# Kernel tuning notes

Hardware: AMD Instinct MI355X
Metric: run time of the kernel (lower is better)

Reference implementation:

```python
import jax, jax.numpy as jnp
import numpy as np

B, CH, H, W = 8, 1024, 64, 64
FD = 128            # feature_dim
NUM_K, POOL_PER_K = 64, 32
POOL = NUM_K * POOL_PER_K  # 2048


def setup_inputs() -> dict:
    key = jax.random.key(0)
    ks = jax.random.split(key, 7)
    s = 0.02  # keep logits in a sane range for softmax
    return {
        "x": jax.random.normal(ks[0], (B, CH, H, W), jnp.float32),
        "w_theta": jax.random.normal(ks[1], (FD, CH), jnp.float32) * s,
        "w_phi": jax.random.normal(ks[2], (FD, CH), jnp.float32) * s,
        "w_g": jax.random.normal(ks[3], (FD, CH), jnp.float32) * s,
        "w_o": jax.random.normal(ks[4], (CH, FD), jnp.float32) * s,
        "gamma": jnp.ones((1,), jnp.float32),
        "concept_pool": jax.random.uniform(ks[5], (FD, POOL), jnp.float32),
    }


def reference(x, w_theta, w_phi, w_g, w_o, gamma, concept_pool):
    b, c, h, w = x.shape
    n = h * w
    xf = x.reshape(b, c, n)                                   # [B, C, N]
    # 1x1 conv projections as matmuls
    theta = jnp.einsum('fc,bcn->bfn', w_theta, xf)            # [B, FD, N]
    # --- concept-codebook cross attention: queries attend over pool entries ---
    cp_logits = jnp.einsum('bfn,fp->bnp', theta, concept_pool)  # [B, N, P]
    cp_attn = jax.nn.softmax(cp_logits, axis=-1)
    pooled = jnp.einsum('bnp,fp->bfn', cp_attn, concept_pool)   # [B, FD, N]
    # --- standard self-attention branch (use_sa=True) ---
    phi = jnp.einsum('fc,bcn->bfn', w_phi, xf)                # [B, FD, N]
    g = jnp.einsum('fc,bcn->bfn', w_g, xf)                    # [B, FD, N]
    sa_logits = jnp.einsum('bfn,bfm->bnm', theta, phi)        # [B, N, N]
    sa_attn = jax.nn.softmax(sa_logits, axis=-1)
    sa_out = jnp.einsum('bnm,bfm->bfn', sa_attn, g)           # [B, FD, N]
    # combine, output 1x1 conv, gamma-scaled residual
    feat = pooled + sa_out
    out = jnp.einsum('cf,bfn->bcn', w_o, feat).reshape(b, c, h, w)
    return gamma[0] * out + x
```

## Files before the change

### kernel.cpp

```cpp
#include <hip/hip_runtime.h>

typedef unsigned short u16;
typedef unsigned int u32;
typedef float f32x4 __attribute__((ext_vector_type(4)));
typedef short s16x8 __attribute__((ext_vector_type(8)));

#define B_ 8
#define C_ 1024
#define N_ 4096
#define FD_ 128
#define P_ 2048
#define LOG2E 1.4426950408889634f

__device__ __forceinline__ u16 f2bf(float f) {
  u32 u = __float_as_uint(f);
  u32 r = (u + 0x7fffu + ((u >> 16) & 1u)) >> 16;
  return (u16)r;
}
__device__ __forceinline__ u32 pkbf(float a, float b) {
  u32 r;
  asm("v_cvt_pk_bf16_f32 %0, %1, %2" : "=v"(r) : "v"(a), "v"(b));
  return r;
}
__device__ __forceinline__ float lo16(u32 u) { return __uint_as_float(u << 16); }
__device__ __forceinline__ float hi16(u32 u) { return __uint_as_float(u & 0xffff0000u); }
__device__ __forceinline__ float bf2f(u16 u) { return __uint_as_float(((u32)u) << 16); }

#define AS1 __attribute__((address_space(1)))
#define AS3 __attribute__((address_space(3)))
__device__ __forceinline__ void gl16(const void* g, void* l) {
  __builtin_amdgcn_global_load_lds((AS1 const u32*)g, (AS3 u32*)l, 16, 0, 0);
}

__device__ __forceinline__ int tau32(int c) {
  return ((c & 4) << 2) + ((c & 24) >> 1) + (c & 3);
}

__global__ __launch_bounds__(256) void prep_kernel(
    const float* __restrict__ wth, const float* __restrict__ wph,
    const float* __restrict__ wg, const float* __restrict__ wo,
    const float* __restrict__ pool,
    u16* __restrict__ wcat, u16* __restrict__ wo_bf,
    u16* __restrict__ pool_k, u16* __restrict__ pool_vt) {
  int idx = blockIdx.x * 256 + threadIdx.x;
  if (idx < 393216) {
    int o = idx;
    int e = o & 7, hi2 = (o >> 3) & 3, lo2 = (o >> 5) & 15;
    int ft = (o >> 9) & 7, ks = (o >> 12) & 1, kk2 = (o >> 13) & 15;
    int y = o >> 17;
    int c = kk2 * 64 + ks * 32 + hi2 * 8 + e;
    int fj = y * 128 + ft * 16 + lo2;
    float v = (fj < 128) ? wth[fj * 1024 + c]
              : (fj < 256 ? wph[(fj - 128) * 1024 + c]
                          : wg[(fj - 256) * 1024 + c]);
    wcat[idx] = f2bf(v);
  } else if (idx < 524288) {
    int i = idx - 393216;
    wo_bf[i] = f2bf(wo[i]);
  } else if (idx < 786432) {
    int i = idx - 524288;
    int p = i >> 7, f = i & 127;
    pool_k[i] = f2bf(pool[f * 2048 + p]);
  } else if (idx < 1048576) {
    int j = idx - 786432;
    int tile = j >> 12, r = j & 4095;
    int ch = r >> 10, f = (r >> 3) & 127, kk = r & 7;
    pool_vt[j] = f2bf(pool[f * 2048 + tile * 32 + tau32(ch * 8 + kk)]);
  }
}

#define SWZ(r) ((((r) + ((r) >> 3)) & 7) << 4)
__global__ __launch_bounds__(256, 2) void proj_kernel(
    const float* __restrict__ x, const u16* __restrict__ wcat,
    u16* __restrict__ q_t, u16* __restrict__ k_t, u16* __restrict__ gvt) {
  __shared__ __align__(16) char sm[34816];
  float* ot = (float*)sm;
  const int tid = threadIdx.x;
  const int w = tid >> 6, lane = tid & 63, lo = lane & 15, hi = lane >> 4;
  const int bid = blockIdx.x;
  const int xcd = bid & 7, slot = bid >> 3;
  const int y = slot % 3, t8 = slot / 3;
  const int tile = t8 * 8 + xcd;
  const int b = tile >> 5, n0 = (tile & 31) * 128;

  const float* xb = x + (size_t)b * (C_ * N_) + n0;
  const u16* wy = wcat + y * 131072;
  const int cq = tid >> 4, nq = tid & 15;

  f32x4 acc[2][8];
#pragma unroll
  for (int s = 0; s < 2; ++s)
#pragma unroll
    for (int ft = 0; ft < 8; ++ft)
#pragma unroll
      for (int j = 0; j < 4; ++j) acc[s][ft][j] = 0.f;

  float4 xa[8];
  s16x8 bA[8], bB[8];

#define LOADX(c0)                                                        \
  {                                                                      \
    _Pragma("unroll") for (int i = 0; i < 4; ++i) {                      \
      const float* p = xb + (size_t)((c0) + cq * 4 + i) * N_ + nq * 8;   \
      xa[i * 2] = *(const float4*)p;                                     \
      xa[i * 2 + 1] = *(const float4*)(p + 4);                           \
    }                                                                    \
  }
#define STOREA(bufsel)                                                   \
  {                                                                      \
    char* ab = sm + (bufsel)*16384;                                      \
    _Pragma("unroll") for (int j = 0; j < 8; ++j) {                      \
      float v0 = xa[0 + (j >> 2)][j & 3];                                \
      float v1 = xa[2 + (j >> 2)][j & 3];                                \
      float v2 = xa[4 + (j >> 2)][j & 3];                                \
      float v3 = xa[6 + (j >> 2)][j & 3];                                \
      uint2 pk;                                                          \
      pk.x = pkbf(v0, v1);                                               \
      pk.y = pkbf(v2, v3);                                               \
      int r = nq * 8 + j;                                                \
      *(uint2*)(ab + r * 128 + ((cq * 8) ^ SWZ(r))) = pk;                \
    }                                                                    \
  }
#define LOADB(dst, kk2, ks)                                              \
  {                                                                      \
    _Pragma("unroll") for (int ft = 0; ft < 8; ++ft) dst[ft] =           \
        *(const s16x8*)(wy + (((kk2)*2 + (ks)) * 8 + ft) * 512 +         \
                        lo * 32 + hi * 8);                               \
  }
#define COMPUTE(bufsel, ks, bf)                                          \
  {                                                                      \
    const char* ab = sm + (bufsel)*16384;                                \
    _Pragma("unroll") for (int s = 0; s < 2; ++s) {                      \
      int r = w * 32 + s * 16 + lo;                                      \
      s16x8 af = *(const s16x8*)(ab + r * 128 +                          \
                                 (((ks)*64 + hi * 16) ^ SWZ(r)));        \
      _Pragma("unroll") for (int ft = 0; ft < 8; ++ft) acc[s][ft] =      \
          __builtin_amdgcn_mfma_f32_16x16x32_bf16(af, bf[ft],            \
                                                  acc[s][ft], 0, 0, 0);  \
    }                                                                    \
  }

  LOADX(0);
  LOADB(bA, 0, 0);
  STOREA(0);
  __syncthreads();

  for (int k = 0; k < 16; ++k) {
    if (k < 15) LOADX((k + 1) * 64);
    LOADB(bB, k, 1);
    COMPUTE(k & 1, 0, bA);
    if (k < 15) LOADB(bA, k + 1, 0);
    COMPUTE(k & 1, 1, bB);
    if (k < 15) STOREA((k & 1) ^ 1);
    __syncthreads();
  }

  const float sc = (y == 0) ? LOG2E : 1.f;
#pragma unroll
  for (int hn = 0; hn < 2; ++hn) {
    if ((w >> 1) == hn) {
#pragma unroll
      for (int s = 0; s < 2; ++s)
#pragma unroll
        for (int ft = 0; ft < 8; ++ft)
#pragma unroll
          for (int j = 0; j < 4; ++j)
            ot[((w & 1) * 32 + s * 16 + hi * 4 + j) * 136 + ft * 16 + lo] =
                acc[s][ft][j] * sc;
    }
    __syncthreads();
    if (y < 2) {
      u16* arr = (y == 0) ? q_t : k_t;
      const int row = tid >> 2, fc = (tid & 3) * 32;
      u16* dst = arr + (size_t)(b * N_ + n0 + hn * 64 + row) * FD_ + fc;
      const float* sp = ot + row * 136 + fc;
#pragma unroll
      for (int k2 = 0; k2 < 4; ++k2) {
        s16x8 vv;
#pragma unroll
        for (int i = 0; i < 8; ++i) vv[i] = (short)f2bf(sp[k2 * 8 + i]);
        *(s16x8*)(dst + k2 * 8) = vv;
      }
    } else {
      const int f = tid >> 1, sel = tid & 1;
      const int t2 = (n0 >> 5) + hn * 2 + sel;
      u16* dstb = gvt + ((size_t)(b * 128 + t2) * 4) * 1024;
#pragma unroll
      for (int ch = 0; ch < 4; ++ch) {
        s16x8 vv;
#pragma unroll
        for (int kk = 0; kk < 8; ++kk) {
          int row = sel * 32 + tau32(ch * 8 + kk);
          vv[kk] = (short)f2bf(ot[row * 136 + f]);
        }
        *(s16x8*)(dstb + (ch * 128 + f) * 8) = vv;
      }
    }
    __syncthreads();
  }
#undef LOADX
#undef STOREA
#undef LOADB
#undef COMPUTE
}

__global__ __launch_bounds__(256, 3) void attn_kernel(
    const u16* __restrict__ q_t, const u16* __restrict__ k_t,
    const u16* __restrict__ pool_k, const u16* __restrict__ pool_vt,
    const u16* __restrict__ gvt, u16* __restrict__ feat1,
    u16* __restrict__ pooled, u16* __restrict__ po1, u16* __restrict__ po2,
    float* __restrict__ lse, const int NS) {
  __shared__ __align__(16) char smem[32768];
  char* kB = smem;
  char* vB = smem + 16384;

  const int tid = threadIdx.x;
  const int w = tid >> 6, lane = tid & 63, lo = lane & 15, hi = lane >> 4;
  const int b = blockIdx.x & 7;
  const int nt = (blockIdx.x >> 3) & 31;
  const int sid = (int)(blockIdx.x >> 8);
  const int n0 = nt * 128;
  const int ntiles = (NS == 3) ? 64 : 192;
  const bool DOPOOL = (NS == 1);

  const int k_dr = lane >> 4, k_cb = (lane & 15) * 16;
  const int sw = (lo & 7) << 4;

  const char* ktb = (const char*)(k_t + (size_t)b * N_ * FD_);
  const char* vtb = (const char*)(gvt + (size_t)b * 128 * 4096);
  const char* kseg0;
  const char* vseg0;
  const char* kseg1 = ktb;
  const char* vseg1 = vtb;
  if (NS == 3 && sid > 0) {
    kseg0 = ktb + (size_t)(sid - 1) * 64 * 8192;
    vseg0 = vtb + (size_t)(sid - 1) * 64 * 8192;
  } else {
    kseg0 = (const char*)pool_k;
    vseg0 = (const char*)pool_vt;
  }

  s16x8 q[2][4];
#pragma unroll
  for (int qf = 0; qf < 2; ++qf) {
    const u16* qbase = q_t + (size_t)(b * N_ + n0 + w * 32 + qf * 16 + lo) * FD_;
#pragma unroll
    for (int kk = 0; kk < 4; ++kk) q[qf][kk] = *(const s16x8*)(qbase + kk * 32 + hi * 8);
  }

  float m_r = -__builtin_inff();
  float l_r[2] = {0.f, 0.f};
  f32x4 o[2][8];
  u32 o1p[2][8][2];
#pragma unroll
  for (int qf = 0; qf < 2; ++qf)
#pragma unroll
    for (int ft = 0; ft < 8; ++ft) {
#pragma unroll
      for (int j = 0; j < 4; ++j) o[qf][ft][j] = 0.f;
      o1p[qf][ft][0] = 0u;
      o1p[qf][ft][1] = 0u;
    }

#define STAGE(i, bufsel)                                                   \
  {                                                                        \
    const char* kg = ((i) < 64) ? kseg0 + (size_t)(i)*8192                 \
                                : kseg1 + (size_t)((i)-64) * 8192;         \
    const char* vg = ((i) < 64) ? vseg0 + (size_t)(i)*8192                 \
                                : vseg1 + (size_t)((i)-64) * 8192;         \
    char* kl = kB + (bufsel)*8192;                                         \
    char* vl = vB + (bufsel)*8192;                                         \
    _Pragma("unroll") for (int cc2 = 0; cc2 < 2; ++cc2) {                  \
      int c = w * 2 + cc2;                                                 \
      int rl = c * 4 + k_dr;                                               \
      gl16(kg + rl * 256 + (k_cb ^ ((rl & 7) << 4)), kl + c * 1024);       \
      gl16(vg + c * 1024 + lane * 16, vl + c * 1024);                      \
    }                                                                      \
  }

  STAGE(0, 0);
  __syncthreads();

  int buf = 0;
  for (int i = 0; i < ntiles; ++i) {
    if (i + 1 < ntiles) STAGE(i + 1, buf ^ 1);
    if (DOPOOL && i == 64) {
#pragma unroll
      for (int qf = 0; qf < 2; ++qf) {
        float lq = l_r[qf];
        lq += __shfl_xor(lq, 16);
        lq += __shfl_xor(lq, 32);
        float inv = __builtin_amdgcn_rcpf(lq);
#pragma unroll
        for (int ft = 0; ft < 8; ++ft) {
          o1p[qf][ft][0] = pkbf(o[qf][ft][0] * inv, o[qf][ft][1] * inv);
          o1p[qf][ft][1] = pkbf(o[qf][ft][2] * inv, o[qf][ft][3] * inv);
#pragma unroll
          for (int j = 0; j < 4; ++j) o[qf][ft][j] = 0.f;
        }
        l_r[qf] = 0.f;
      }
      m_r = -__builtin_inff();
    }

    const char* kbc = kB + buf * 8192;
    const char* vbc = vB + buf * 8192;

    f32x4 s[2][2];
#pragma unroll
    for (int qf = 0; qf < 2; ++qf)
#pragma unroll
      for (int t = 0; t < 2; ++t)
#pragma unroll
        for (int j = 0; j < 4; ++j) s[qf][t][j] = 0.f;
#pragma unroll
    for (int kk = 0; kk < 4; ++kk) {
      const int cb = (kk * 64 + hi * 16) ^ sw;
      s16x8 kf0 = *(const s16x8*)(kbc + lo * 256 + cb);
      s16x8 kf1 = *(const s16x8*)(kbc + (16 + lo) * 256 + cb);
#pragma unroll
      for (int qf = 0; qf < 2; ++qf) {
        s[qf][0] = __builtin_amdgcn_mfma_f32_16x16x32_bf16(kf0, q[qf][kk], s[qf][0], 0, 0, 0);
        s[qf][1] = __builtin_amdgcn_mfma_f32_16x16x32_bf16(kf1, q[qf][kk], s[qf][1], 0, 0, 0);
      }
    }
    float tm = fmaxf(
        fmaxf(fmaxf(fmaxf(s[0][0][0], s[0][0][1]), fmaxf(s[0][0][2], s[0][0][3])),
              fmaxf(fmaxf(s[0][1][0], s[0][1][1]), fmaxf(s[0][1][2], s[0][1][3]))),
        fmaxf(fmaxf(fmaxf(s[1][0][0], s[1][0][1]), fmaxf(s[1][0][2], s[1][0][3])),
              fmaxf(fmaxf(s[1][1][0], s[1][1][1]), fmaxf(s[1][1][2], s[1][1][3]))));
    tm = fmaxf(tm, __shfl_xor(tm, 16));
    tm = fmaxf(tm, __shfl_xor(tm, 32));
    if (__any(tm - m_r > 11.5f)) {
      float mn = fmaxf(m_r, tm);
      float al = exp2f(m_r - mn);
      m_r = mn;
      l_r[0] *= al;
      l_r[1] *= al;
#pragma unroll
      for (int qf = 0; qf < 2; ++qf)
#pragma unroll
        for (int ft = 0; ft < 8; ++ft)
#pragma unroll
          for (int j = 0; j < 4; ++j) o[qf][ft][j] *= al;
    }
    union Frag { u32 u[4]; s16x8 v; };
    Frag pb[2];
#pragma unroll
    for (int qf = 0; qf < 2; ++qf) {
      float rs = 0.f;
#pragma unroll
      for (int t = 0; t < 2; ++t)
#pragma unroll
        for (int j = 0; j < 4; ++j) {
          float p = exp2f(s[qf][t][j] - m_r);
          s[qf][t][j] = p;
          rs += p;
        }
      l_r[qf] += rs;
      pb[qf].u[0] = pkbf(s[qf][0][0], s[qf][0][1]);
      pb[qf].u[1] = pkbf(s[qf][0][2], s[qf][0][3]);
      pb[qf].u[2] = pkbf(s[qf][1][0], s[qf][1][1]);
      pb[qf].u[3] = pkbf(s[qf][1][2], s[qf][1][3]);
    }
#pragma unroll
    for (int ft = 0; ft < 8; ++ft) {
      const int f = ft * 16 + lo;
      s16x8 vf = *(const s16x8*)(vbc + hi * 2048 + f * 16);
      o[0][ft] = __builtin_amdgcn_mfma_f32_16x16x32_bf16(vf, pb[0].v, o[0][ft], 0, 0, 0);
      o[1][ft] = __builtin_amdgcn_mfma_f32_16x16x32_bf16(vf, pb[1].v, o[1][ft], 0, 0, 0);
    }
    __syncthreads();
    buf ^= 1;
  }
#undef STAGE

#pragma unroll
  for (int qf = 0; qf < 2; ++qf) {
    float lq = l_r[qf];
    lq += __shfl_xor(lq, 16);
    lq += __shfl_xor(lq, 32);
    float inv = __builtin_amdgcn_rcpf(lq);
    const size_t row = (size_t)(b * N_ + n0 + w * 32 + qf * 16 + lo);
    if (NS == 1) {
#pragma unroll
      for (int ft = 0; ft < 8; ++ft) {
        float v0 = lo16(o1p[qf][ft][0]) + o[qf][ft][0] * inv;
        float v1 = hi16(o1p[qf][ft][0]) + o[qf][ft][1] * inv;
        float v2 = lo16(o1p[qf][ft][1]) + o[qf][ft][2] * inv;
        float v3 = hi16(o1p[qf][ft][1]) + o[qf][ft][3] * inv;
        uint2 st = {pkbf(v0, v1), pkbf(v2, v3)};
        *(uint2*)(feat1 + row * FD_ + ft * 16 + hi * 4) = st;
      }
    } else {
      u16* dst = (sid == 0) ? pooled : ((sid == 1) ? po1 : po2);
#pragma unroll
      for (int ft = 0; ft < 8; ++ft) {
        uint2 st = {pkbf(o[qf][ft][0] * inv, o[qf][ft][1] * inv),
                    pkbf(o[qf][ft][2] * inv, o[qf][ft][3] * inv)};
        *(uint2*)(dst + row * FD_ + ft * 16 + hi * 4) = st;
      }
      if (sid > 0 && hi == 0) lse[(sid - 1) * 32768 + row] = m_r + log2f(lq);
    }
  }
}

__global__ __launch_bounds__(256) void merge_kernel(
    const u16* __restrict__ pooled, const u16* __restrict__ po1,
    const u16* __restrict__ po2, const float* __restrict__ lse,
    u16* __restrict__ featq) {
  const int tid = threadIdx.x;
  const int n = blockIdx.x * 32 + (tid >> 3);
  const int fc = (tid & 7) * 16;
  float l1 = lse[n], l2 = lse[32768 + n];
  float mx = fmaxf(l1, l2);
  float w1 = exp2f(l1 - mx), w2 = exp2f(l2 - mx);
  float dn = __builtin_amdgcn_rcpf(w1 + w2);
  float a1 = w1 * dn, a2 = w2 * dn;
  const size_t base = (size_t)n * FD_ + fc;
#pragma unroll
  for (int h = 0; h < 2; ++h) {
    s16x8 xp = *(const s16x8*)(pooled + base + h * 8);
    s16x8 x1 = *(const s16x8*)(po1 + base + h * 8);
    s16x8 x2 = *(const s16x8*)(po2 + base + h * 8);
    s16x8 r;
#pragma unroll
    for (int i = 0; i < 8; ++i) {
      float v = bf2f((u16)xp[i]) + bf2f((u16)x1[i]) * a1 + bf2f((u16)x2[i]) * a2;
      r[i] = (short)f2bf(v);
    }
    *(s16x8*)(featq + base + h * 8) = r;
  }
}

__global__ __launch_bounds__(256) void final_kernel(
    const float* __restrict__ x, const u16* __restrict__ wo_bf,
    const u16* __restrict__ feat, const float* __restrict__ gamma,
    float* __restrict__ out) {
  __shared__ __align__(16) char sm[17408];
  float* fl = (float*)sm;
  const int tid = threadIdx.x;
  const int w = tid >> 6, lane = tid & 63, lo = lane & 15, hi = lane >> 4;
  const int n0 = blockIdx.x * 64, c0 = blockIdx.y * 64, b = blockIdx.z;

  {
    const char* fb = (const char*)(feat + (size_t)(b * N_ + n0) * FD_);
#pragma unroll
    for (int r2 = 0; r2 < 4; ++r2) {
      int off = r2 * 4096 + tid * 16;
      int row = off >> 8, colb = off & 255;
      gl16(fb + row * 256 + (colb ^ ((row & 7) << 4)), sm + off);
    }
  }
  const u16* arow = wo_bf + (c0 + w * 16 + lo) * FD_ + hi * 8;
  s16x8 af[4];
#pragma unroll
  for (int kk = 0; kk < 4; ++kk) af[kk] = *(const s16x8*)(arow + kk * 32);

  f32x4 acc[4];
#pragma unroll
  for (int i = 0; i < 4; ++i)
#pragma unroll
    for (int j = 0; j < 4; ++j) acc[i][j] = 0.f;

  __syncthreads();

  const int swf = (lo & 7) << 4;
#pragma unroll
  for (int kk = 0; kk < 4; ++kk)
#pragma unroll
    for (int nt = 0; nt < 4; ++nt) {
      const int row = nt * 16 + lo;
      s16x8 bf = *(const s16x8*)(sm + row * 256 + ((kk * 64 + hi * 16) ^ swf));
      acc[nt] = __builtin_amdgcn_mfma_f32_16x16x32_bf16(af[kk], bf, acc[nt], 0, 0, 0);
    }

  __syncthreads();
#pragma unroll
  for (int nt = 0; nt < 4; ++nt)
#pragma unroll
    for (int j = 0; j < 4; ++j)
      fl[(w * 16 + hi * 4 + j) * 68 + nt * 16 + lo] = acc[nt][j];
  __syncthreads();
  const float gm = gamma[0];
  const int cl = tid >> 2, nc = (tid & 3) * 16;
  const size_t xo = (size_t)b * C_ * N_ + (size_t)(c0 + cl) * N_ + n0 + nc;
  const float* sp = fl + cl * 68 + nc;
#pragma unroll
  for (int k2 = 0; k2 < 4; ++k2) {
    float4 v = *(const float4*)(sp + k2 * 4);
    float4 xi = *(const float4*)(x + xo + k2 * 4);
    float4 r;
    r.x = gm * v.x + xi.x;
    r.y = gm * v.y + xi.y;
    r.z = gm * v.z + xi.z;
    r.w = gm * v.w + xi.w;
    *(float4*)(out + xo + k2 * 4) = r;
  }
}

extern "C" void kernel_launch(void* const* d_in, const int* in_sizes, int n_in,
                              void* d_out, int out_size, void* d_ws, size_t ws_size,
                              hipStream_t stream) {
  const float* x = (const float*)d_in[0];
  const float* wth = (const float*)d_in[1];
  const float* wph = (const float*)d_in[2];
  const float* wg = (const float*)d_in[3];
  const float* wo = (const float*)d_in[4];
  const float* gamma = (const float*)d_in[5];
  const float* pool = (const float*)d_in[6];
  float* out = (float*)d_out;

  char* ws = (char*)d_ws;
  u16* wcat    = (u16*)(ws + 0);
  u16* wo_bf   = (u16*)(ws + 786432);
  u16* pool_k  = (u16*)(ws + 1048576);
  u16* pool_vt = (u16*)(ws + 1572864);
  u16* q_t     = (u16*)(ws + 2097152);
  u16* k_t     = (u16*)(ws + 10485760);
  u16* gvt     = (u16*)(ws + 18874368);
  u16* feat1   = (u16*)(ws + 27262976);
  u16* pooled  = (u16*)(ws + 27262976);
  u16* po1     = (u16*)(ws + 35651584);
  u16* po2     = (u16*)(ws + 44040192);
  float* lse   = (float*)(ws + 52428800);
  u16* featq   = q_t;
  const size_t NEED = 52690944ull;
  const int NS = (ws_size >= NEED) ? 3 : 1;

  prep_kernel<<<4096, 256, 0, stream>>>(wth, wph, wg, wo, pool, wcat, wo_bf, pool_k, pool_vt);
  proj_kernel<<<768, 256, 0, stream>>>(x, wcat, q_t, k_t, gvt);
  attn_kernel<<<(NS == 3) ? 768 : 256, 256, 0, stream>>>(
      q_t, k_t, pool_k, pool_vt, gvt, feat1, pooled, po1, po2, lse, NS);
  const u16* featp = feat1;
  if (NS == 3) {
    merge_kernel<<<1024, 256, 0, stream>>>(pooled, po1, po2, lse, featq);
    featp = featq;
  }
  final_kernel<<<dim3(64, 16, 8), 256, 0, stream>>>(x, wo_bf, featp, gamma, out);
}
```

Measured before the change: 267.4 us.

## Drop LDS staging in attention and read K/V tiles directly from global

```diff
diff --git a/kernel.cpp b/kernel.cpp
--- a/kernel.cpp
+++ b/kernel.cpp
@@ -204,27 +204,20 @@
 #undef COMPUTE
 }
 
-__global__ __launch_bounds__(256, 3) void attn_kernel(
+__global__ __launch_bounds__(64, 4) void attn_kernel(
     const u16* __restrict__ q_t, const u16* __restrict__ k_t,
     const u16* __restrict__ pool_k, const u16* __restrict__ pool_vt,
     const u16* __restrict__ gvt, u16* __restrict__ feat1,
     u16* __restrict__ pooled, u16* __restrict__ po1, u16* __restrict__ po2,
     float* __restrict__ lse, const int NS) {
-  __shared__ __align__(16) char smem[32768];
-  char* kB = smem;
-  char* vB = smem + 16384;
-
-  const int tid = threadIdx.x;
-  const int w = tid >> 6, lane = tid & 63, lo = lane & 15, hi = lane >> 4;
+  const int lane = threadIdx.x;
+  const int lo = lane & 15, hi = lane >> 4;
   const int b = blockIdx.x & 7;
-  const int nt = (blockIdx.x >> 3) & 31;
-  const int sid = (int)(blockIdx.x >> 8);
-  const int n0 = nt * 128;
+  const int nt = (blockIdx.x >> 3) & 127;
+  const int sid = (int)(blockIdx.x >> 10);
+  const int n0 = nt * 32;
   const int ntiles = (NS == 3) ? 64 : 192;
   const bool DOPOOL = (NS == 1);
-
-  const int k_dr = lane >> 4, k_cb = (lane & 15) * 16;
-  const int sw = (lo & 7) << 4;
 
   const char* ktb = (const char*)(k_t + (size_t)b * N_ * FD_);
   const char* vtb = (const char*)(gvt + (size_t)b * 128 * 4096);
@@ -243,7 +236,7 @@
   s16x8 q[2][4];
 #pragma unroll
   for (int qf = 0; qf < 2; ++qf) {
-    const u16* qbase = q_t + (size_t)(b * N_ + n0 + w * 32 + qf * 16 + lo) * FD_;
+    const u16* qbase = q_t + (size_t)(b * N_ + n0 + qf * 16 + lo) * FD_;
 #pragma unroll
     for (int kk = 0; kk < 4; ++kk) q[qf][kk] = *(const s16x8*)(qbase + kk * 32 + hi * 8);
   }
@@ -262,28 +255,7 @@
       o1p[qf][ft][1] = 0u;
     }
 
-#define STAGE(i, bufsel)                                                   \
-  {                                                                        \
-    const char* kg = ((i) < 64) ? kseg0 + (size_t)(i)*8192                 \
-                                : kseg1 + (size_t)((i)-64) * 8192;         \
-    const char* vg = ((i) < 64) ? vseg0 + (size_t)(i)*8192                 \
-                                : vseg1 + (size_t)((i)-64) * 8192;         \
-    char* kl = kB + (bufsel)*8192;                                         \
-    char* vl = vB + (bufsel)*8192;                                         \
-    _Pragma("unroll") for (int cc2 = 0; cc2 < 2; ++cc2) {                  \
-      int c = w * 2 + cc2;                                                 \
-      int rl = c * 4 + k_dr;                                               \
-      gl16(kg + rl * 256 + (k_cb ^ ((rl & 7) << 4)), kl + c * 1024);       \
-      gl16(vg + c * 1024 + lane * 16, vl + c * 1024);                      \
-    }                                                                      \
-  }
-
-  STAGE(0, 0);
-  __syncthreads();
-
-  int buf = 0;
   for (int i = 0; i < ntiles; ++i) {
-    if (i + 1 < ntiles) STAGE(i + 1, buf ^ 1);
     if (DOPOOL && i == 64) {
 #pragma unroll
       for (int qf = 0; qf < 2; ++qf) {
@@ -303,8 +275,10 @@
       m_r = -__builtin_inff();
     }
 
-    const char* kbc = kB + buf * 8192;
-    const char* vbc = vB + buf * 8192;
+    const char* kbc = (i < 64) ? kseg0 + (size_t)i * 8192
+                               : kseg1 + (size_t)(i - 64) * 8192;
+    const char* vbc = (i < 64) ? vseg0 + (size_t)i * 8192
+                               : vseg1 + (size_t)(i - 64) * 8192;
 
     f32x4 s[2][2];
 #pragma unroll
@@ -315,7 +289,7 @@
         for (int j = 0; j < 4; ++j) s[qf][t][j] = 0.f;
 #pragma unroll
     for (int kk = 0; kk < 4; ++kk) {
-      const int cb = (kk * 64 + hi * 16) ^ sw;
+      const int cb = kk * 64 + hi * 16;
       s16x8 kf0 = *(const s16x8*)(kbc + lo * 256 + cb);
       s16x8 kf1 = *(const s16x8*)(kbc + (16 + lo) * 256 + cb);
 #pragma unroll
@@ -370,10 +344,7 @@
       o[0][ft] = __builtin_amdgcn_mfma_f32_16x16x32_bf16(vf, pb[0].v, o[0][ft], 0, 0, 0);
       o[1][ft] = __builtin_amdgcn_mfma_f32_16x16x32_bf16(vf, pb[1].v, o[1][ft], 0, 0, 0);
     }
-    __syncthreads();
-    buf ^= 1;
-  }
-#undef STAGE
+  }
 
 #pragma unroll
   for (int qf = 0; qf < 2; ++qf) {
@@ -381,7 +352,7 @@
     lq += __shfl_xor(lq, 16);
     lq += __shfl_xor(lq, 32);
     float inv = __builtin_amdgcn_rcpf(lq);
-    const size_t row = (size_t)(b * N_ + n0 + w * 32 + qf * 16 + lo);
+    const size_t row = (size_t)(b * N_ + n0 + qf * 16 + lo);
     if (NS == 1) {
 #pragma unroll
       for (int ft = 0; ft < 8; ++ft) {
@@ -530,7 +501,7 @@
 
   prep_kernel<<<4096, 256, 0, stream>>>(wth, wph, wg, wo, pool, wcat, wo_bf, pool_k, pool_vt);
   proj_kernel<<<768, 256, 0, stream>>>(x, wcat, q_t, k_t, gvt);
-  attn_kernel<<<(NS == 3) ? 768 : 256, 256, 0, stream>>>(
+  attn_kernel<<<(NS == 3) ? 3072 : 1024, 64, 0, stream>>>(
       q_t, k_t, pool_k, pool_vt, gvt, feat1, pooled, po1, po2, lse, NS);
   const u16* featp = feat1;
   if (NS == 3) {
```

Measured after the change: 483.1 us. 1.81x slower.

## Split attention into five segments with finer split-K and MFMA priority hints

Applied to the files above, without the earlier changes.

```diff
diff --git a/kernel.cpp b/kernel.cpp
--- a/kernel.cpp
+++ b/kernel.cpp
@@ -204,12 +204,11 @@
 #undef COMPUTE
 }
 
-__global__ __launch_bounds__(256, 3) void attn_kernel(
+__global__ __launch_bounds__(256, 5) void attn_kernel(
     const u16* __restrict__ q_t, const u16* __restrict__ k_t,
     const u16* __restrict__ pool_k, const u16* __restrict__ pool_vt,
     const u16* __restrict__ gvt, u16* __restrict__ feat1,
-    u16* __restrict__ pooled, u16* __restrict__ po1, u16* __restrict__ po2,
-    float* __restrict__ lse, const int NS) {
+    u16* __restrict__ parts, float* __restrict__ lse, const int NSEG) {
   __shared__ __align__(16) char smem[32768];
   char* kB = smem;
   char* vB = smem + 16384;
@@ -220,8 +219,7 @@
   const int nt = (blockIdx.x >> 3) & 31;
   const int sid = (int)(blockIdx.x >> 8);
   const int n0 = nt * 128;
-  const int ntiles = (NS == 3) ? 64 : 192;
-  const bool DOPOOL = (NS == 1);
+  const bool DOPOOL = (NSEG == 1);
 
   const int k_dr = lane >> 4, k_cb = (lane & 15) * 16;
   const int sw = (lo & 7) << 4;
@@ -230,14 +228,27 @@
   const char* vtb = (const char*)(gvt + (size_t)b * 128 * 4096);
   const char* kseg0;
   const char* vseg0;
-  const char* kseg1 = ktb;
-  const char* vseg1 = vtb;
-  if (NS == 3 && sid > 0) {
-    kseg0 = ktb + (size_t)(sid - 1) * 64 * 8192;
-    vseg0 = vtb + (size_t)(sid - 1) * 64 * 8192;
+  const char* kseg1;
+  const char* vseg1;
+  int tcnt;
+  if (NSEG == 5) {
+    switch (sid) {
+      case 0:  kseg0 = (const char*)pool_k; vseg0 = (const char*)pool_vt; tcnt = 32; break;
+      case 1:  kseg0 = (const char*)pool_k + 262144; vseg0 = (const char*)pool_vt + 262144; tcnt = 32; break;
+      case 2:  kseg0 = ktb;            vseg0 = vtb;            tcnt = 43; break;
+      case 3:  kseg0 = ktb + 352256;   vseg0 = vtb + 352256;   tcnt = 43; break;
+      default: kseg0 = ktb + 704512;   vseg0 = vtb + 704512;   tcnt = 42; break;
+    }
+    kseg1 = kseg0 + 524288; vseg1 = vseg0 + 524288;
+  } else if (NSEG == 3) {
+    if (sid == 0) { kseg0 = (const char*)pool_k; vseg0 = (const char*)pool_vt; }
+    else { kseg0 = ktb + (size_t)(sid - 1) * 524288; vseg0 = vtb + (size_t)(sid - 1) * 524288; }
+    kseg1 = kseg0 + 524288; vseg1 = vseg0 + 524288;
+    tcnt = 64;
   } else {
-    kseg0 = (const char*)pool_k;
-    vseg0 = (const char*)pool_vt;
+    kseg0 = (const char*)pool_k; vseg0 = (const char*)pool_vt;
+    kseg1 = ktb; vseg1 = vtb;
+    tcnt = 192;
   }
 
   s16x8 q[2][4];
@@ -282,8 +293,8 @@
   __syncthreads();
 
   int buf = 0;
-  for (int i = 0; i < ntiles; ++i) {
-    if (i + 1 < ntiles) STAGE(i + 1, buf ^ 1);
+  for (int i = 0; i < tcnt; ++i) {
+    if (i + 1 < tcnt) STAGE(i + 1, buf ^ 1);
     if (DOPOOL && i == 64) {
 #pragma unroll
       for (int qf = 0; qf < 2; ++qf) {
@@ -313,6 +324,7 @@
       for (int t = 0; t < 2; ++t)
 #pragma unroll
         for (int j = 0; j < 4; ++j) s[qf][t][j] = 0.f;
+    __builtin_amdgcn_s_setprio(1);
 #pragma unroll
     for (int kk = 0; kk < 4; ++kk) {
       const int cb = (kk * 64 + hi * 16) ^ sw;
@@ -324,14 +336,15 @@
         s[qf][1] = __builtin_amdgcn_mfma_f32_16x16x32_bf16(kf1, q[qf][kk], s[qf][1], 0, 0, 0);
       }
     }
-    float tm = fmaxf(
+    __builtin_amdgcn_s_setprio(0);
+    float lm = fmaxf(
         fmaxf(fmaxf(fmaxf(s[0][0][0], s[0][0][1]), fmaxf(s[0][0][2], s[0][0][3])),
               fmaxf(fmaxf(s[0][1][0], s[0][1][1]), fmaxf(s[0][1][2], s[0][1][3]))),
         fmaxf(fmaxf(fmaxf(s[1][0][0], s[1][0][1]), fmaxf(s[1][0][2], s[1][0][3])),
               fmaxf(fmaxf(s[1][1][0], s[1][1][1]), fmaxf(s[1][1][2], s[1][1][3]))));
-    tm = fmaxf(tm, __shfl_xor(tm, 16));
-    tm = fmaxf(tm, __shfl_xor(tm, 32));
-    if (__any(tm - m_r > 11.5f)) {
+    if (__any(lm - m_r > 11.5f)) {
+      float tm = fmaxf(lm, __shfl_xor(lm, 16));
+      tm = fmaxf(tm, __shfl_xor(tm, 32));
       float mn = fmaxf(m_r, tm);
       float al = exp2f(m_r - mn);
       m_r = mn;
@@ -363,6 +376,7 @@
       pb[qf].u[2] = pkbf(s[qf][1][0], s[qf][1][1]);
       pb[qf].u[3] = pkbf(s[qf][1][2], s[qf][1][3]);
     }
+    __builtin_amdgcn_s_setprio(1);
 #pragma unroll
     for (int ft = 0; ft < 8; ++ft) {
       const int f = ft * 16 + lo;
@@ -370,6 +384,7 @@
       o[0][ft] = __builtin_amdgcn_mfma_f32_16x16x32_bf16(vf, pb[0].v, o[0][ft], 0, 0, 0);
       o[1][ft] = __builtin_amdgcn_mfma_f32_16x16x32_bf16(vf, pb[1].v, o[1][ft], 0, 0, 0);
     }
+    __builtin_amdgcn_s_setprio(0);
     __syncthreads();
     buf ^= 1;
   }
@@ -382,7 +397,7 @@
     lq += __shfl_xor(lq, 32);
     float inv = __builtin_amdgcn_rcpf(lq);
     const size_t row = (size_t)(b * N_ + n0 + w * 32 + qf * 16 + lo);
-    if (NS == 1) {
+    if (NSEG == 1) {
 #pragma unroll
       for (int ft = 0; ft < 8; ++ft) {
         float v0 = lo16(o1p[qf][ft][0]) + o[qf][ft][0] * inv;
@@ -393,21 +408,23 @@
         *(uint2*)(feat1 + row * FD_ + ft * 16 + hi * 4) = st;
       }
     } else {
-      u16* dst = (sid == 0) ? pooled : ((sid == 1) ? po1 : po2);
+      u16* dst = parts + (size_t)sid * 4194304;
 #pragma unroll
       for (int ft = 0; ft < 8; ++ft) {
         uint2 st = {pkbf(o[qf][ft][0] * inv, o[qf][ft][1] * inv),
                     pkbf(o[qf][ft][2] * inv, o[qf][ft][3] * inv)};
         *(uint2*)(dst + row * FD_ + ft * 16 + hi * 4) = st;
       }
-      if (sid > 0 && hi == 0) lse[(sid - 1) * 32768 + row] = m_r + log2f(lq);
-    }
-  }
-}
-
-__global__ __launch_bounds__(256) void merge_kernel(
-    const u16* __restrict__ pooled, const u16* __restrict__ po1,
-    const u16* __restrict__ po2, const float* __restrict__ lse,
+      if ((NSEG == 5 || sid > 0) && hi == 0) {
+        int lslot = (NSEG == 5) ? sid : sid - 1;
+        lse[lslot * 32768 + row] = m_r + log2f(lq);
+      }
+    }
+  }
+}
+
+__global__ __launch_bounds__(256) void merge3_kernel(
+    const u16* __restrict__ parts, const float* __restrict__ lse,
     u16* __restrict__ featq) {
   const int tid = threadIdx.x;
   const int n = blockIdx.x * 32 + (tid >> 3);
@@ -420,13 +437,49 @@
   const size_t base = (size_t)n * FD_ + fc;
 #pragma unroll
   for (int h = 0; h < 2; ++h) {
-    s16x8 xp = *(const s16x8*)(pooled + base + h * 8);
-    s16x8 x1 = *(const s16x8*)(po1 + base + h * 8);
-    s16x8 x2 = *(const s16x8*)(po2 + base + h * 8);
+    s16x8 xp = *(const s16x8*)(parts + base + h * 8);
+    s16x8 x1 = *(const s16x8*)(parts + 4194304 + base + h * 8);
+    s16x8 x2 = *(const s16x8*)(parts + 8388608 + base + h * 8);
     s16x8 r;
 #pragma unroll
     for (int i = 0; i < 8; ++i) {
       float v = bf2f((u16)xp[i]) + bf2f((u16)x1[i]) * a1 + bf2f((u16)x2[i]) * a2;
+      r[i] = (short)f2bf(v);
+    }
+    *(s16x8*)(featq + base + h * 8) = r;
+  }
+}
+
+__global__ __launch_bounds__(256) void merge5_kernel(
+    const u16* __restrict__ parts, const float* __restrict__ lse,
+    u16* __restrict__ featq) {
+  const int tid = threadIdx.x;
+  const int n = blockIdx.x * 32 + (tid >> 3);
+  const int fc = (tid & 7) * 16;
+  float l0 = lse[n], l1 = lse[32768 + n];
+  float l2 = lse[65536 + n], l3 = lse[98304 + n], l4 = lse[131072 + n];
+  float mp = fmaxf(l0, l1);
+  float w0 = exp2f(l0 - mp), w1 = exp2f(l1 - mp);
+  float dp = __builtin_amdgcn_rcpf(w0 + w1);
+  float a0 = w0 * dp, a1 = w1 * dp;
+  float ms = fmaxf(fmaxf(l2, l3), l4);
+  float w2 = exp2f(l2 - ms), w3 = exp2f(l3 - ms), w4 = exp2f(l4 - ms);
+  float ds = __builtin_amdgcn_rcpf(w2 + w3 + w4);
+  float a2 = w2 * ds, a3 = w3 * ds, a4 = w4 * ds;
+  const size_t base = (size_t)n * FD_ + fc;
+#pragma unroll
+  for (int h = 0; h < 2; ++h) {
+    s16x8 p0 = *(const s16x8*)(parts + base + h * 8);
+    s16x8 p1 = *(const s16x8*)(parts + 4194304 + base + h * 8);
+    s16x8 p2 = *(const s16x8*)(parts + 8388608 + base + h * 8);
+    s16x8 p3 = *(const s16x8*)(parts + 12582912 + base + h * 8);
+    s16x8 p4 = *(const s16x8*)(parts + 16777216 + base + h * 8);
+    s16x8 r;
+#pragma unroll
+    for (int i = 0; i < 8; ++i) {
+      float v = bf2f((u16)p0[i]) * a0 + bf2f((u16)p1[i]) * a1 +
+                bf2f((u16)p2[i]) * a2 + bf2f((u16)p3[i]) * a3 +
+                bf2f((u16)p4[i]) * a4;
       r[i] = (short)f2bf(v);
     }
     *(s16x8*)(featq + base + h * 8) = r;
@@ -519,23 +572,26 @@
   u16* q_t     = (u16*)(ws + 2097152);
   u16* k_t     = (u16*)(ws + 10485760);
   u16* gvt     = (u16*)(ws + 18874368);
+  u16* parts   = (u16*)(ws + 27262976);
   u16* feat1   = (u16*)(ws + 27262976);
-  u16* pooled  = (u16*)(ws + 27262976);
-  u16* po1     = (u16*)(ws + 35651584);
-  u16* po2     = (u16*)(ws + 44040192);
-  float* lse   = (float*)(ws + 52428800);
   u16* featq   = q_t;
-  const size_t NEED = 52690944ull;
-  const int NS = (ws_size >= NEED) ? 3 : 1;
+
+  const size_t NEED5 = 69861376ull;
+  const size_t NEED3 = 52690944ull;
+  const int NSEG = (ws_size >= NEED5) ? 5 : (ws_size >= NEED3) ? 3 : 1;
+  float* lse = (NSEG == 5) ? (float*)(ws + 69206016) : (float*)(ws + 52428800);
 
   prep_kernel<<<4096, 256, 0, stream>>>(wth, wph, wg, wo, pool, wcat, wo_bf, pool_k, pool_vt);
   proj_kernel<<<768, 256, 0, stream>>>(x, wcat, q_t, k_t, gvt);
-  attn_kernel<<<(NS == 3) ? 768 : 256, 256, 0, stream>>>(
-      q_t, k_t, pool_k, pool_vt, gvt, feat1, pooled, po1, po2, lse, NS);
+  attn_kernel<<<(NSEG == 5) ? 1280 : (NSEG == 3) ? 768 : 256, 256, 0, stream>>>(
+      q_t, k_t, pool_k, pool_vt, gvt, feat1, parts, lse, NSEG);
   const u16* featp = feat1;
-  if (NS == 3) {
-    merge_kernel<<<1024, 256, 0, stream>>>(pooled, po1, po2, lse, featq);
+  if (NSEG == 5) {
+    merge5_kernel<<<1024, 256, 0, stream>>>(parts, lse, featq);
     featp = featq;
+  } else if (NSEG == 3) {
+    merge3_kernel<<<1024, 256, 0, stream>>>(parts, lse, featq);
+    featp = featq;
   }
   final_kernel<<<dim3(64, 16, 8), 256, 0, stream>>>(x, wo_bf, featp, gamma, out);
 }
```

Measured after the change: 722.0 us. 170% more time.
